# Kernel tuning notes

Hardware: AMD Instinct MI355X
Metric: run time of the kernel (lower is better)

The kernel has to match this reference:

```python
import jax, jax.numpy as jnp
import numpy as np

LORA_RANK = 16
LORA_ALPHA = 32
CHUNK_SIZE = 256
TTT_LR = 0.01
CLIP_THRESHOLD = 1.0
SCALING = LORA_ALPHA / LORA_RANK
LN_EPS = 1e-5


def setup_inputs() -> dict:
    key = jax.random.key(0)
    ks = jax.random.split(key, 5)
    B, S, K, H = 2, 8192, 1024, 1024
    x = jax.random.normal(ks[0], (B, S, K), dtype=jnp.float32)
    Wb = jax.random.normal(ks[1], (H, K), dtype=jnp.float32) / np.sqrt(K)
    init_A = jax.random.normal(ks[2], (H, LORA_RANK), dtype=jnp.float32) * 0.01
    init_B = jax.random.normal(ks[3], (LORA_RANK, K), dtype=jnp.float32) * 0.01
    ln_gamma = jnp.ones((K,), dtype=jnp.float32)
    ln_beta = jnp.zeros((K,), dtype=jnp.float32)
    Wp = jax.random.normal(ks[4], (H, K), dtype=jnp.float32) / np.sqrt(K)
    return {"x": x, "Wb": Wb, "init_A": init_A, "init_B": init_B,
            "ln_gamma": ln_gamma, "ln_beta": ln_beta, "Wp": Wp}


def _forward(x, Wb, init_A, init_B, ln_gamma, ln_beta, Wp):
    B_sz, Seq, k_dim = x.shape
    h_dim = Wb.shape[0]
    r = init_A.shape[1]
    nc = Seq // CHUNK_SIZE  # Seq chosen divisible; pad_len == 0

    base_out = x @ Wb.T  # [B, S, H]

    # --- target construction under no_grad: LayerNorm + left-shift ---
    xd = jax.lax.stop_gradient(x)
    mu = jnp.mean(xd, axis=-1, keepdims=True)
    var = jnp.mean((xd - mu) ** 2, axis=-1, keepdims=True)
    xn = (xd - mu) * jax.lax.rsqrt(var + LN_EPS) * ln_gamma + ln_beta
    shifted = jnp.pad(xn[:, 1:, :], ((0, 0), (0, 1), (0, 0)))
    shifted = jax.lax.stop_gradient(shifted)

    V = shifted @ Wp.T  # [B, S, H]

    Z = x.reshape(B_sz * nc, CHUNK_SIZE, k_dim)
    Vc = V.reshape(B_sz * nc, CHUNK_SIZE, h_dim)

    # per-chunk fast-weight deltas
    proj_in = Z @ init_B.T                                # [BC, C, r]
    dA = jnp.einsum('bch,bcr->bhr', Vc, proj_in)          # [BC, H, r]
    proj_err = Vc @ init_A                                # [BC, C, r]
    dB = jnp.einsum('bcr,bck->brk', proj_err, Z)          # [BC, r, K]

    dA = dA.reshape(B_sz, nc, h_dim, r)
    dB = dB.reshape(B_sz, nc, r, k_dim)

    # exclusive cross-chunk cumsum
    accA = jnp.cumsum(dA, axis=1)
    accB = jnp.cumsum(dB, axis=1)
    accA = jnp.concatenate([jnp.zeros_like(accA[:, :1]), accA[:, :-1]], axis=1)
    accB = jnp.concatenate([jnp.zeros_like(accB[:, :1]), accB[:, :-1]], axis=1)

    lr = TTT_LR * SCALING
    rawA = (lr * accA).reshape(-1, h_dim, r)
    rawB = (lr * accB).reshape(-1, r, k_dim)

    # joint norm clip (norm_type=2)
    norm_sq = (jnp.sum(rawA.astype(jnp.float32) ** 2, axis=(-2, -1), keepdims=True)
               + jnp.sum(rawB.astype(jnp.float32) ** 2, axis=(-2, -1), keepdims=True))
    total_norm = jnp.sqrt(norm_sq)
    coef = jnp.minimum(CLIP_THRESHOLD / (total_norm + 1e-6), 1.0).astype(rawA.dtype)

    A_eff = init_A[None] - rawA * coef  # [BC, H, r]
    B_eff = init_B[None] - rawB * coef  # [BC, r, K]

    mid = jnp.einsum('bck,brk->bcr', Z, B_eff)          # [BC, C, r]
    lora = jnp.einsum('bcr,bhr->bch', mid, A_eff)       # [BC, C, H]
    lora = lora.reshape(B_sz, Seq, h_dim)

    return base_out + lora * SCALING


def reference(x, Wb, init_A, init_B, ln_gamma, ln_beta, Wp):
    return _forward(x, Wb, init_A, init_B, ln_gamma, ln_beta, Wp)
```

## Files before the change

### kernel.cpp

```cpp
#include <hip/hip_runtime.h>

typedef __attribute__((ext_vector_type(8))) short s16x8;
typedef __attribute__((ext_vector_type(4))) float f32x4;
typedef __attribute__((ext_vector_type(2))) float f32x2;
typedef unsigned short u16;

#define B_SZ 2
#define SEQ 8192
#define KD 1024
#define HD 1024
#define RK 16
#define CH 256
#define NCH 64
static constexpr float LR_SC = 0.02f;
static constexpr float SCALE_OUT = 2.0f;

__device__ __forceinline__ u16 f2b(float f) {
  union { float f; unsigned int u; } c; c.f = f;
  unsigned int u = c.u;
  unsigned int r = (u + 0x7fffu + ((u >> 16) & 1u)) >> 16;
  return (u16)r;
}
__device__ __forceinline__ float b2f(u16 v) {
  union { unsigned int u; float f; } c; c.u = ((unsigned int)v) << 16; return c.f;
}
__device__ __forceinline__ void async16(const u16* g, u16* l) {
  __builtin_amdgcn_global_load_lds((const __attribute__((address_space(1))) void*)g,
                                   (__attribute__((address_space(3))) void*)l, 16, 0, 0);
}

__global__ __launch_bounds__(256) void cvt_all(const float* __restrict__ Wb,
                                               const float* __restrict__ Wp,
                                               const float* __restrict__ initB,
                                               u16* __restrict__ Wbb,
                                               u16* __restrict__ Wpb,
                                               u16* __restrict__ iBb) {
  int bid = blockIdx.x;
  const float* src; u16* dst; int base;
  if (bid < 1024)      { src = Wb;    dst = Wbb; base = bid; }
  else if (bid < 2048) { src = Wp;    dst = Wpb; base = bid - 1024; }
  else                 { src = initB; dst = iBb; base = bid - 2048; }
  int i = (base * 256 + threadIdx.x) * 4;
  float4 v = *(const float4*)(src + i);
  ushort4 o; o.x = f2b(v.x); o.y = f2b(v.y); o.z = f2b(v.z); o.w = f2b(v.w);
  *(ushort4*)(dst + i) = o;
}

__global__ __launch_bounds__(256) void wpat_part(const float* __restrict__ initA,
                                                 const float* __restrict__ Wp,
                                                 float* __restrict__ part) {
  int t = threadIdx.x;
  int k = blockIdx.x * 256 + t;
  int hseg = blockIdx.y;
  __shared__ float Asm[64 * 16];
  *(float4*)&Asm[t * 4] = *(const float4*)&initA[(size_t)hseg * 1024 + t * 4];
  __syncthreads();
  float acc[16];
  #pragma unroll
  for (int j = 0; j < 16; j++) acc[j] = 0.f;
  const float* wp = Wp + (size_t)hseg * 64 * KD + k;
  #pragma unroll 8
  for (int hh = 0; hh < 64; hh++) {
    float w = wp[(size_t)hh * KD];
    const float4* ar = (const float4*)&Asm[hh * 16];
    #pragma unroll
    for (int qq = 0; qq < 4; qq++) {
      float4 a = ar[qq];
      acc[qq*4+0] += w * a.x; acc[qq*4+1] += w * a.y;
      acc[qq*4+2] += w * a.z; acc[qq*4+3] += w * a.w;
    }
  }
  float* o = part + ((size_t)hseg * 1024 + k) * 16;
  #pragma unroll
  for (int qq = 0; qq < 4; qq++) {
    float4 r; r.x = acc[qq*4]; r.y = acc[qq*4+1]; r.z = acc[qq*4+2]; r.w = acc[qq*4+3];
    *(float4*)&o[qq * 4] = r;
  }
}

__global__ __launch_bounds__(256) void wpat_reduce(const float* __restrict__ part,
                                                   u16* __restrict__ WpAT) {
  int idx = blockIdx.x * 256 + threadIdx.x;
  int k = idx & 1023, r = idx >> 10;
  float s = 0.f;
  #pragma unroll
  for (int seg = 0; seg < 16; seg++)
    s += part[((size_t)seg * 1024 + k) * 16 + r];
  WpAT[(size_t)r * KD + k] = f2b(s);
}

__global__ __launch_bounds__(256) void ln_shift(const float* __restrict__ x,
                                                const float* __restrict__ gamma,
                                                const float* __restrict__ beta,
                                                u16* __restrict__ xb,
                                                u16* __restrict__ shb) {
  int row = blockIdx.x;
  int t = threadIdx.x;
  int s = row & (SEQ - 1);
  const float* xr = x + (size_t)row * KD;
  float4 v = *(const float4*)(xr + t * 4);
  ushort4 o; o.x = f2b(v.x); o.y = f2b(v.y); o.z = f2b(v.z); o.w = f2b(v.w);
  *(ushort4*)(xb + (size_t)row * KD + t * 4) = o;

  if (s == 0) {
    ushort4 z; z.x = 0; z.y = 0; z.z = 0; z.w = 0;
    *(ushort4*)(shb + ((size_t)row + SEQ - 1) * KD + t * 4) = z;
    return;
  }
  float s1 = v.x + v.y + v.z + v.w;
  float s2 = v.x * v.x + v.y * v.y + v.z * v.z + v.w * v.w;
  #pragma unroll
  for (int off = 32; off > 0; off >>= 1) {
    s1 += __shfl_down(s1, off);
    s2 += __shfl_down(s2, off);
  }
  __shared__ float red[8];
  int wave = t >> 6, lane = t & 63;
  if (lane == 0) { red[wave * 2] = s1; red[wave * 2 + 1] = s2; }
  __syncthreads();
  float sum = red[0] + red[2] + red[4] + red[6];
  float ssq = red[1] + red[3] + red[5] + red[7];
  float mu = sum * (1.0f / KD);
  float var = ssq * (1.0f / KD) - mu * mu;
  float rstd = rsqrtf(var + 1e-5f);
  float4 g = *(const float4*)(gamma + t * 4);
  float4 bb = *(const float4*)(beta + t * 4);
  ushort4 so;
  so.x = f2b((v.x - mu) * rstd * g.x + bb.x);
  so.y = f2b((v.y - mu) * rstd * g.y + bb.y);
  so.z = f2b((v.z - mu) * rstd * g.z + bb.z);
  so.w = f2b((v.w - mu) * rstd * g.w + bb.w);
  *(ushort4*)(shb + (size_t)(row - 1) * KD + t * 4) = so;
}

__global__ __launch_bounds__(256, 2) void gemm_fused(const u16* __restrict__ A,
                                                     const u16* __restrict__ Bm,
                                                     const u16* __restrict__ mid2,
                                                     const u16* __restrict__ Aef,
                                                     float* __restrict__ C) {
  constexpr int BM = 128, BN = 128, BK = 64, N = HD, Kd = KD;
  __shared__ __align__(16) char SMEMRAW[64 * 132 * 4];
  u16* As = (u16*)SMEMRAW;
  u16* Bs = (u16*)(SMEMRAW + BM * BK * 2);
  float* SM = (float*)SMEMRAW;
  int tid = threadIdx.x;
  int lane = tid & 63, wave = tid >> 6;
  int lb = blockIdx.x + 8 * blockIdx.y;
  int q = lb & 7, t = lb >> 3;
  int mb = q * 16 + (t >> 3);
  int nb = t & 7;
  int m0 = mb * 128, n0 = nb * 128;
  int wm = (wave >> 1) * 64, wn = (wave & 1) * 64;
  int lr = lane & 15;
  int qd = lane >> 4;
  int sw = lr & 7;
  int slot0 = ((qd ^ sw) * 8);
  int slot1 = (((4 + qd) ^ sw) * 8);
  f32x4 acc[4][4] = {};

  const u16* gbase; u16* lbase;
  if (wave < 2) { gbase = A + (size_t)(m0 + wave * 64) * Kd; lbase = As + wave * 64 * BK; }
  else          { gbase = Bm + (size_t)(n0 + (wave - 2) * 64) * Kd; lbase = Bs + (wave - 2) * 64 * BK; }
  int srow = lane >> 3;
  int scol = ((lane & 7) ^ srow) * 8;
  const u16* gsrc = gbase + (size_t)srow * Kd + scol;

  for (int k0 = 0; k0 < Kd; k0 += BK) {
    #pragma unroll
    for (int i = 0; i < 8; i++)
      async16(gsrc + (size_t)i * 8 * Kd, lbase + i * 512);
    gsrc += BK;
    __syncthreads();
    s16x8 af[4], bfr[4];
    #pragma unroll
    for (int i = 0; i < 4; i++) af[i] = *(const s16x8*)(As + (wm + i * 16 + lr) * BK + slot0);
    #pragma unroll
    for (int j = 0; j < 4; j++) bfr[j] = *(const s16x8*)(Bs + (wn + j * 16 + lr) * BK + slot0);
    #pragma unroll
    for (int i = 0; i < 4; i++)
      #pragma unroll
      for (int j = 0; j < 4; j++)
        acc[i][j] = __builtin_amdgcn_mfma_f32_16x16x32_bf16(af[i], bfr[j], acc[i][j], 0, 0, 0);
    #pragma unroll
    for (int i = 0; i < 4; i++) af[i] = *(const s16x8*)(As + (wm + i * 16 + lr) * BK + slot1);
    #pragma unroll
    for (int j = 0; j < 4; j++) bfr[j] = *(const s16x8*)(Bs + (wn + j * 16 + lr) * BK + slot1);
    #pragma unroll
    for (int i = 0; i < 4; i++)
      #pragma unroll
      for (int j = 0; j < 4; j++)
        acc[i][j] = __builtin_amdgcn_mfma_f32_16x16x32_bf16(af[i], bfr[j], acc[i][j], 0, 0, 0);
    __syncthreads();
  }

  {
    int chunk = m0 >> 8;
    const u16* abase = Aef + (size_t)chunk * (HD * RK);
    int klane = lane >> 4;
    s16x8 am2[4], bn2[4];
    #pragma unroll
    for (int i = 0; i < 4; i++) {
      if (klane < 2)
        am2[i] = *(const s16x8*)(mid2 + (size_t)(m0 + wm + i * 16 + lr) * RK + klane * 8);
      else { s16x8 z = {}; am2[i] = z; }
    }
    #pragma unroll
    for (int j = 0; j < 4; j++) {
      if (klane < 2)
        bn2[j] = *(const s16x8*)(abase + (size_t)(n0 + wn + j * 16 + lr) * RK + klane * 8);
      else { s16x8 z = {}; bn2[j] = z; }
    }
    #pragma unroll
    for (int i = 0; i < 4; i++)
      #pragma unroll
      for (int j = 0; j < 4; j++)
        acc[i][j] = __builtin_amdgcn_mfma_f32_16x16x32_bf16(am2[i], bn2[j], acc[i][j], 0, 0, 0);
  }

  int rb = qd * 4, cc = lr;
  int row8 = tid >> 3;
  int fidx = tid & 7;
  #pragma unroll
  for (int h = 0; h < 2; h++) {
    __syncthreads();
    if ((wave >> 1) == h) {
      #pragma unroll
      for (int i = 0; i < 4; i++)
        #pragma unroll
        for (int j = 0; j < 4; j++)
          #pragma unroll
          for (int p = 0; p < 4; p++)
            SM[(i * 16 + rb + p) * 132 + wn + j * 16 + cc] = acc[i][j][p];
    }
    __syncthreads();
    #pragma unroll
    for (int s = 0; s < 2; s++) {
      int rl = s * 32 + row8;
      const float* src = SM + rl * 132 + fidx * 4;
      float* dst = C + (size_t)(m0 + h * 64 + rl) * N + n0 + fidx * 4;
      #pragma unroll
      for (int qq = 0; qq < 4; qq++)
        *(float4*)(dst + qq * 32) = *(const float4*)(src + qq * 32);
    }
  }
}

__global__ __launch_bounds__(256) void rank16_proj(const u16* __restrict__ xb,
                                                   const u16* __restrict__ shb,
                                                   const u16* __restrict__ iBb,
                                                   const u16* __restrict__ WpAT,
                                                   float* __restrict__ pin,
                                                   float* __restrict__ per) {
  const u16* X; const u16* W; float* O;
  if (blockIdx.z == 0) { X = xb; W = iBb; O = pin; }
  else                 { X = shb; W = WpAT; O = per; }
  int wave = threadIdx.x >> 6, lane = threadIdx.x & 63;
  int m0 = (blockIdx.x * 4 + wave) * 16;
  int lr = lane & 15, lk = (lane >> 4) * 8;
  const u16* xp = X + (size_t)(m0 + lr) * KD + lk;
  const u16* wp = W + (size_t)lr * KD + lk;
  f32x4 acc = {};
  #pragma unroll 8
  for (int k0 = 0; k0 < KD; k0 += 32) {
    s16x8 a = *(const s16x8*)xp;
    s16x8 b = *(const s16x8*)wp;
    acc = __builtin_amdgcn_mfma_f32_16x16x32_bf16(a, b, acc, 0, 0, 0);
    xp += 32; wp += 32;
  }
  int rb = (lane >> 4) * 4, cc = lane & 15;
  #pragma unroll
  for (int p = 0; p < 4; p++)
    O[(size_t)(m0 + rb + p) * RK + cc] = acc[p];
}

__global__ __launch_bounds__(256) void rank16_mid(const u16* __restrict__ xb,
                                                  const u16* __restrict__ Bef,
                                                  u16* __restrict__ mid2) {
  int wave = threadIdx.x >> 6, lane = threadIdx.x & 63;
  int m0 = (blockIdx.x * 4 + wave) * 16;
  int chunk = m0 >> 8;
  int lr = lane & 15, lk = (lane >> 4) * 8;
  const u16* xp = xb + (size_t)(m0 + lr) * KD + lk;
  const u16* wp = Bef + (size_t)chunk * (RK * KD) + (size_t)lr * KD + lk;
  f32x4 acc = {};
  #pragma unroll 8
  for (int k0 = 0; k0 < KD; k0 += 32) {
    s16x8 a = *(const s16x8*)xp;
    s16x8 b = *(const s16x8*)wp;
    acc = __builtin_amdgcn_mfma_f32_16x16x32_bf16(a, b, acc, 0, 0, 0);
    xp += 32; wp += 32;
  }
  int rb = (lane >> 4) * 4, cc = lane & 15;
  #pragma unroll
  for (int p = 0; p < 4; p++)
    mid2[(size_t)(m0 + rb + p) * RK + cc] = f2b(SCALE_OUT * acc[p]);
}

__global__ __launch_bounds__(256) void gk_kernel(const u16* __restrict__ xb,
                                                 const u16* __restrict__ shb,
                                                 const float* __restrict__ pin,
                                                 const float* __restrict__ per,
                                                 float* __restrict__ G,
                                                 float* __restrict__ dB) {
  int tile = blockIdx.x;
  int chunk = blockIdx.y;
  int which = blockIdx.z;
  int t = threadIdx.x;
  __shared__ float P[CH * RK];
  const float* psrc = which ? per : pin;
  for (int i = t; i < 1024; i += 256)
    *(float4*)&P[i * 4] = *(const float4*)&psrc[(size_t)chunk * 4096 + i * 4];
  __syncthreads();
  f32x2 acc[8];
  #pragma unroll
  for (int j = 0; j < 8; j++) acc[j] = (f32x2){0.f, 0.f};
  int col = tile * 256 + t;
  const u16* src = (which ? xb : shb) + (size_t)chunk * CH * KD + col;
  #pragma unroll 4
  for (int c = 0; c < 256; c++) {
    float v = b2f(src[(size_t)c * 1024]);
    f32x2 vv = {v, v};
    const f32x2* pr = (const f32x2*)&P[c * 16];
    #pragma unroll
    for (int qq = 0; qq < 8; qq++)
      acc[qq] += vv * pr[qq];
  }
  float* o = (which ? dB : G) + (size_t)chunk * 16384 + col;
  #pragma unroll
  for (int j = 0; j < 8; j++) {
    o[(size_t)(2 * j) * 1024] = acc[j][0];
    o[(size_t)(2 * j + 1) * 1024] = acc[j][1];
  }
}

__global__ __launch_bounds__(256) void cumsum_kernel(const float* __restrict__ G,
                                                     const float* __restrict__ dB,
                                                     u16* __restrict__ rawG,
                                                     float* __restrict__ rawB) {
  int idx = blockIdx.x * 256 + threadIdx.x;
  int which = idx >> 15;
  int rem = idx & 32767;
  int b = rem >> 14;
  int e = rem & 16383;
  size_t base = (size_t)b * 32 * 16384 + e;
  if (which == 0) {
    float run = 0.f;
    #pragma unroll 8
    for (int i = 0; i < 32; i++) {
      size_t off = base + (size_t)i * 16384;
      float nv = G[off];
      rawG[off] = f2b(LR_SC * run);
      run += nv;
    }
  } else {
    float run = 0.f;
    #pragma unroll 8
    for (int i = 0; i < 32; i++) {
      size_t off = base + (size_t)i * 16384;
      float nv = dB[off];
      rawB[off] = LR_SC * run;
      run += nv;
    }
  }
}

__global__ __launch_bounds__(256) void dagemm(const u16* __restrict__ Wpb,
                                              const u16* __restrict__ rawG,
                                              float* __restrict__ rawA) {
  int wave = threadIdx.x >> 6, lane = threadIdx.x & 63;
  int m0 = (blockIdx.x * 4 + wave) * 16;
  int chunk = blockIdx.y;
  int lr = lane & 15, lk = (lane >> 4) * 8;
  const u16* ap = Wpb + (size_t)(m0 + lr) * KD + lk;
  const u16* bp = rawG + (size_t)chunk * 16384 + (size_t)lr * KD + lk;
  f32x4 acc = {};
  #pragma unroll 8
  for (int k0 = 0; k0 < KD; k0 += 32) {
    s16x8 a = *(const s16x8*)ap;
    s16x8 b = *(const s16x8*)bp;
    acc = __builtin_amdgcn_mfma_f32_16x16x32_bf16(a, b, acc, 0, 0, 0);
    ap += 32; bp += 32;
  }
  int rb = (lane >> 4) * 4, cc = lane & 15;
  #pragma unroll
  for (int p = 0; p < 4; p++)
    rawA[(size_t)chunk * 16384 + (size_t)(m0 + rb + p) * RK + cc] = acc[p];
}

__global__ __launch_bounds__(256) void coef_norm(const float* __restrict__ rawA,
                                                 const float* __restrict__ rawB,
                                                 float* __restrict__ part) {
  int b = blockIdx.x;
  int chunk = b >> 2, quarter = b & 3;
  size_t base = (size_t)chunk * 16384 + quarter * 4096;
  const float* a = rawA + base;
  const float* bb = rawB + base;
  int t = threadIdx.x;
  float s = 0.f;
  #pragma unroll
  for (int i = 0; i < 4; i++) {
    float4 v = *(const float4*)(a + (i * 256 + t) * 4);
    s += v.x*v.x + v.y*v.y + v.z*v.z + v.w*v.w;
    float4 w = *(const float4*)(bb + (i * 256 + t) * 4);
    s += w.x*w.x + w.y*w.y + w.z*w.z + w.w*w.w;
  }
  #pragma unroll
  for (int off = 32; off > 0; off >>= 1) s += __shfl_down(s, off);
  __shared__ float red[4];
  int wave = t >> 6, lane = t & 63;
  if (lane == 0) red[wave] = s;
  __syncthreads();
  if (t == 0) part[b] = red[0] + red[1] + red[2] + red[3];
}

__global__ __launch_bounds__(256) void coef_emit(const float* __restrict__ initA,
                                                 const float* __restrict__ initB,
                                                 const float* __restrict__ rawA,
                                                 const float* __restrict__ rawB,
                                                 const float* __restrict__ part,
                                                 u16* __restrict__ Aef,
                                                 u16* __restrict__ Bef) {
  int b = blockIdx.x;
  int chunk = b >> 3, eighth = b & 7;
  float tot = part[chunk * 4] + part[chunk * 4 + 1] + part[chunk * 4 + 2] + part[chunk * 4 + 3];
  float cf = fminf(1.0f / (sqrtf(tot) + 1e-6f), 1.0f);
  size_t cbase = (size_t)chunk * 16384;
  int t = threadIdx.x;
  #pragma unroll
  for (int i = 0; i < 2; i++) {
    int idx = eighth * 2048 + (i * 256 + t) * 4;
    float4 iv = *(const float4*)(initA + idx);
    float4 rv = *(const float4*)(rawA + cbase + idx);
    ushort4 r;
    r.x = f2b(iv.x - rv.x * cf); r.y = f2b(iv.y - rv.y * cf);
    r.z = f2b(iv.z - rv.z * cf); r.w = f2b(iv.w - rv.w * cf);
    *(ushort4*)(Aef + cbase + idx) = r;
    float4 iw = *(const float4*)(initB + idx);
    float4 rw = *(const float4*)(rawB + cbase + idx);
    ushort4 rr;
    rr.x = f2b(iw.x - rw.x * cf); rr.y = f2b(iw.y - rw.y * cf);
    rr.z = f2b(iw.z - rw.z * cf); rr.w = f2b(iw.w - rw.w * cf);
    *(ushort4*)(Bef + cbase + idx) = rr;
  }
}

extern "C" void kernel_launch(void* const* d_in, const int* in_sizes, int n_in,
                              void* d_out, int out_size, void* d_ws, size_t ws_size,
                              hipStream_t stream) {
  (void)in_sizes; (void)n_in; (void)out_size; (void)ws_size;
  const float* x     = (const float*)d_in[0];
  const float* Wb    = (const float*)d_in[1];
  const float* initA = (const float*)d_in[2];
  const float* initB = (const float*)d_in[3];
  const float* gamma = (const float*)d_in[4];
  const float* beta  = (const float*)d_in[5];
  const float* Wp    = (const float*)d_in[6];
  float* out = (float*)d_out;

  char* ws = (char*)d_ws;
  size_t off = 0;
  auto alloc = [&](size_t bytes) -> void* {
    void* p = ws + off;
    off = (off + bytes + 255) & ~(size_t)255;
    return p;
  };
  const size_t ROWS = (size_t)B_SZ * SEQ;
  u16* xb    = (u16*)alloc(ROWS * KD * 2);
  u16* shb   = (u16*)alloc(ROWS * KD * 2);
  u16* Wbb   = (u16*)alloc((size_t)HD * KD * 2);
  u16* Wpb   = (u16*)alloc((size_t)HD * KD * 2);
  u16* iBb   = (u16*)alloc((size_t)RK * KD * 2);
  u16* WpAT  = (u16*)alloc((size_t)RK * KD * 2);
  float* wpart = (float*)alloc((size_t)16 * KD * RK * 4);
  float* pin = (float*)alloc((size_t)NCH * CH * RK * 4);
  float* per = (float*)alloc((size_t)NCH * CH * RK * 4);
  float* G   = (float*)alloc((size_t)NCH * 16384 * 4);
  float* dB  = (float*)alloc((size_t)NCH * 16384 * 4);
  u16* rawG  = (u16*)alloc((size_t)NCH * 16384 * 2);
  float* rawB= (float*)alloc((size_t)NCH * 16384 * 4);
  float* rawA= (float*)alloc((size_t)NCH * 16384 * 4);
  u16* Aef   = (u16*)alloc((size_t)NCH * 16384 * 2);
  u16* Bef   = (u16*)alloc((size_t)NCH * 16384 * 2);
  u16* mid2  = (u16*)alloc(ROWS * RK * 2);
  float* npart = (float*)alloc((size_t)256 * 4);

  cvt_all<<<2064, 256, 0, stream>>>(Wb, Wp, initB, Wbb, Wpb, iBb);
  wpat_part<<<dim3(4, 16), 256, 0, stream>>>(initA, Wp, wpart);
  wpat_reduce<<<64, 256, 0, stream>>>(wpart, WpAT);
  ln_shift<<<ROWS, 256, 0, stream>>>(x, gamma, beta, xb, shb);
  rank16_proj<<<dim3(256, 1, 2), 256, 0, stream>>>(xb, shb, iBb, WpAT, pin, per);
  gk_kernel<<<dim3(4, NCH, 2), 256, 0, stream>>>(xb, shb, pin, per, G, dB);
  cumsum_kernel<<<256, 256, 0, stream>>>(G, dB, rawG, rawB);
  dagemm<<<dim3(16, NCH), 256, 0, stream>>>(Wpb, rawG, rawA);
  coef_norm<<<256, 256, 0, stream>>>(rawA, rawB, npart);
  coef_emit<<<512, 256, 0, stream>>>(initA, initB, rawA, rawB, npart, Aef, Bef);
  rank16_mid<<<256, 256, 0, stream>>>(xb, Bef, mid2);
  gemm_fused<<<dim3(8, 128), 256, 0, stream>>>(xb, Wbb, mid2, Aef, out);
}
```

Before: 285.4 us.

## Use one wave per row in LayerNorm, dual MFMA accumulators, batched cumsum loads

LayerNorm/shift now processes one row per wavefront with 16 floats per lane and a pure shuffle reduction, removing the shared-memory reduction and block barrier and quartering the block count. The rank-16 MFMA loops split into two independent accumulators to break the dependency chain. The cumsum kernel preloads all 32 values before the scan to expose memory-level parallelism, and gk_kernel's unroll goes from 4 to 8. Register pressure rises in several kernels.

```diff
diff --git a/kernel.cpp b/kernel.cpp
--- a/kernel.cpp
+++ b/kernel.cpp
@@ -27,6 +27,10 @@
 __device__ __forceinline__ void async16(const u16* g, u16* l) {
   __builtin_amdgcn_global_load_lds((const __attribute__((address_space(1))) void*)g,
                                    (__attribute__((address_space(3))) void*)l, 16, 0, 0);
+}
+__device__ __forceinline__ ushort4 cvt4(float4 v) {
+  ushort4 o; o.x = f2b(v.x); o.y = f2b(v.y); o.z = f2b(v.z); o.w = f2b(v.w);
+  return o;
 }
 
 __global__ __launch_bounds__(256) void cvt_all(const float* __restrict__ Wb,
@@ -42,8 +46,7 @@
   else                 { src = initB; dst = iBb; base = bid - 2048; }
   int i = (base * 256 + threadIdx.x) * 4;
   float4 v = *(const float4*)(src + i);
-  ushort4 o; o.x = f2b(v.x); o.y = f2b(v.y); o.z = f2b(v.z); o.w = f2b(v.w);
-  *(ushort4*)(dst + i) = o;
+  *(ushort4*)(dst + i) = cvt4(v);
 }
 
 __global__ __launch_bounds__(256) void wpat_part(const float* __restrict__ initA,
@@ -94,43 +97,64 @@
                                                 const float* __restrict__ beta,
                                                 u16* __restrict__ xb,
                                                 u16* __restrict__ shb) {
-  int row = blockIdx.x;
-  int t = threadIdx.x;
+  int wave = threadIdx.x >> 6, lane = threadIdx.x & 63;
+  int row = blockIdx.x * 4 + wave;
   int s = row & (SEQ - 1);
-  const float* xr = x + (size_t)row * KD;
-  float4 v = *(const float4*)(xr + t * 4);
-  ushort4 o; o.x = f2b(v.x); o.y = f2b(v.y); o.z = f2b(v.z); o.w = f2b(v.w);
-  *(ushort4*)(xb + (size_t)row * KD + t * 4) = o;
+  int col = lane * 16;
+  const float* xr = x + (size_t)row * KD + col;
+  float4 v0 = *(const float4*)(xr + 0);
+  float4 v1 = *(const float4*)(xr + 4);
+  float4 v2 = *(const float4*)(xr + 8);
+  float4 v3 = *(const float4*)(xr + 12);
+  u16* xo = xb + (size_t)row * KD + col;
+  *(ushort4*)(xo + 0)  = cvt4(v0);
+  *(ushort4*)(xo + 4)  = cvt4(v1);
+  *(ushort4*)(xo + 8)  = cvt4(v2);
+  *(ushort4*)(xo + 12) = cvt4(v3);
 
   if (s == 0) {
     ushort4 z; z.x = 0; z.y = 0; z.z = 0; z.w = 0;
-    *(ushort4*)(shb + ((size_t)row + SEQ - 1) * KD + t * 4) = z;
+    u16* zo = shb + ((size_t)row + SEQ - 1) * KD + col;
+    *(ushort4*)(zo + 0) = z; *(ushort4*)(zo + 4) = z;
+    *(ushort4*)(zo + 8) = z; *(ushort4*)(zo + 12) = z;
     return;
   }
-  float s1 = v.x + v.y + v.z + v.w;
-  float s2 = v.x * v.x + v.y * v.y + v.z * v.z + v.w * v.w;
+  float s1 = v0.x+v0.y+v0.z+v0.w + v1.x+v1.y+v1.z+v1.w
+           + v2.x+v2.y+v2.z+v2.w + v3.x+v3.y+v3.z+v3.w;
+  float s2 = v0.x*v0.x+v0.y*v0.y+v0.z*v0.z+v0.w*v0.w
+           + v1.x*v1.x+v1.y*v1.y+v1.z*v1.z+v1.w*v1.w
+           + v2.x*v2.x+v2.y*v2.y+v2.z*v2.z+v2.w*v2.w
+           + v3.x*v3.x+v3.y*v3.y+v3.z*v3.z+v3.w*v3.w;
   #pragma unroll
   for (int off = 32; off > 0; off >>= 1) {
-    s1 += __shfl_down(s1, off);
-    s2 += __shfl_down(s2, off);
-  }
-  __shared__ float red[8];
-  int wave = t >> 6, lane = t & 63;
-  if (lane == 0) { red[wave * 2] = s1; red[wave * 2 + 1] = s2; }
-  __syncthreads();
-  float sum = red[0] + red[2] + red[4] + red[6];
-  float ssq = red[1] + red[3] + red[5] + red[7];
-  float mu = sum * (1.0f / KD);
-  float var = ssq * (1.0f / KD) - mu * mu;
+    s1 += __shfl_xor(s1, off);
+    s2 += __shfl_xor(s2, off);
+  }
+  float mu = s1 * (1.0f / KD);
+  float var = s2 * (1.0f / KD) - mu * mu;
   float rstd = rsqrtf(var + 1e-5f);
-  float4 g = *(const float4*)(gamma + t * 4);
-  float4 bb = *(const float4*)(beta + t * 4);
-  ushort4 so;
-  so.x = f2b((v.x - mu) * rstd * g.x + bb.x);
-  so.y = f2b((v.y - mu) * rstd * g.y + bb.y);
-  so.z = f2b((v.z - mu) * rstd * g.z + bb.z);
-  so.w = f2b((v.w - mu) * rstd * g.w + bb.w);
-  *(ushort4*)(shb + (size_t)(row - 1) * KD + t * 4) = so;
+  float4 g0 = *(const float4*)(gamma + col + 0);
+  float4 g1 = *(const float4*)(gamma + col + 4);
+  float4 g2 = *(const float4*)(gamma + col + 8);
+  float4 g3 = *(const float4*)(gamma + col + 12);
+  float4 b0 = *(const float4*)(beta + col + 0);
+  float4 b1 = *(const float4*)(beta + col + 4);
+  float4 b2 = *(const float4*)(beta + col + 8);
+  float4 b3 = *(const float4*)(beta + col + 12);
+  u16* so = shb + (size_t)(row - 1) * KD + col;
+  float4 r;
+  r.x=(v0.x-mu)*rstd*g0.x+b0.x; r.y=(v0.y-mu)*rstd*g0.y+b0.y;
+  r.z=(v0.z-mu)*rstd*g0.z+b0.z; r.w=(v0.w-mu)*rstd*g0.w+b0.w;
+  *(ushort4*)(so + 0) = cvt4(r);
+  r.x=(v1.x-mu)*rstd*g1.x+b1.x; r.y=(v1.y-mu)*rstd*g1.y+b1.y;
+  r.z=(v1.z-mu)*rstd*g1.z+b1.z; r.w=(v1.w-mu)*rstd*g1.w+b1.w;
+  *(ushort4*)(so + 4) = cvt4(r);
+  r.x=(v2.x-mu)*rstd*g2.x+b2.x; r.y=(v2.y-mu)*rstd*g2.y+b2.y;
+  r.z=(v2.z-mu)*rstd*g2.z+b2.z; r.w=(v2.w-mu)*rstd*g2.w+b2.w;
+  *(ushort4*)(so + 8) = cvt4(r);
+  r.x=(v3.x-mu)*rstd*g3.x+b3.x; r.y=(v3.y-mu)*rstd*g3.y+b3.y;
+  r.z=(v3.z-mu)*rstd*g3.z+b3.z; r.w=(v3.w-mu)*rstd*g3.w+b3.w;
+  *(ushort4*)(so + 12) = cvt4(r);
 }
 
 __global__ __launch_bounds__(256, 2) void gemm_fused(const u16* __restrict__ A,
@@ -259,14 +283,16 @@
   int lr = lane & 15, lk = (lane >> 4) * 8;
   const u16* xp = X + (size_t)(m0 + lr) * KD + lk;
   const u16* wp = W + (size_t)lr * KD + lk;
-  f32x4 acc = {};
+  f32x4 acc0 = {}, acc1 = {};
   #pragma unroll 8
-  for (int k0 = 0; k0 < KD; k0 += 32) {
-    s16x8 a = *(const s16x8*)xp;
-    s16x8 b = *(const s16x8*)wp;
-    acc = __builtin_amdgcn_mfma_f32_16x16x32_bf16(a, b, acc, 0, 0, 0);
-    xp += 32; wp += 32;
-  }
+  for (int k0 = 0; k0 < KD; k0 += 64) {
+    acc0 = __builtin_amdgcn_mfma_f32_16x16x32_bf16(*(const s16x8*)xp,
+                                                   *(const s16x8*)wp, acc0, 0, 0, 0);
+    acc1 = __builtin_amdgcn_mfma_f32_16x16x32_bf16(*(const s16x8*)(xp + 32),
+                                                   *(const s16x8*)(wp + 32), acc1, 0, 0, 0);
+    xp += 64; wp += 64;
+  }
+  f32x4 acc = acc0 + acc1;
   int rb = (lane >> 4) * 4, cc = lane & 15;
   #pragma unroll
   for (int p = 0; p < 4; p++)
@@ -282,14 +308,16 @@
   int lr = lane & 15, lk = (lane >> 4) * 8;
   const u16* xp = xb + (size_t)(m0 + lr) * KD + lk;
   const u16* wp = Bef + (size_t)chunk * (RK * KD) + (size_t)lr * KD + lk;
-  f32x4 acc = {};
+  f32x4 acc0 = {}, acc1 = {};
   #pragma unroll 8
-  for (int k0 = 0; k0 < KD; k0 += 32) {
-    s16x8 a = *(const s16x8*)xp;
-    s16x8 b = *(const s16x8*)wp;
-    acc = __builtin_amdgcn_mfma_f32_16x16x32_bf16(a, b, acc, 0, 0, 0);
-    xp += 32; wp += 32;
-  }
+  for (int k0 = 0; k0 < KD; k0 += 64) {
+    acc0 = __builtin_amdgcn_mfma_f32_16x16x32_bf16(*(const s16x8*)xp,
+                                                   *(const s16x8*)wp, acc0, 0, 0, 0);
+    acc1 = __builtin_amdgcn_mfma_f32_16x16x32_bf16(*(const s16x8*)(xp + 32),
+                                                   *(const s16x8*)(wp + 32), acc1, 0, 0, 0);
+    xp += 64; wp += 64;
+  }
+  f32x4 acc = acc0 + acc1;
   int rb = (lane >> 4) * 4, cc = lane & 15;
   #pragma unroll
   for (int p = 0; p < 4; p++)
@@ -316,7 +344,7 @@
   for (int j = 0; j < 8; j++) acc[j] = (f32x2){0.f, 0.f};
   int col = tile * 256 + t;
   const u16* src = (which ? xb : shb) + (size_t)chunk * CH * KD + col;
-  #pragma unroll 4
+  #pragma unroll 8
   for (int c = 0; c < 256; c++) {
     float v = b2f(src[(size_t)c * 1024]);
     f32x2 vv = {v, v};
@@ -344,22 +372,24 @@
   int e = rem & 16383;
   size_t base = (size_t)b * 32 * 16384 + e;
   if (which == 0) {
+    float v[32];
+    #pragma unroll
+    for (int i = 0; i < 32; i++) v[i] = G[base + (size_t)i * 16384];
     float run = 0.f;
-    #pragma unroll 8
+    #pragma unroll
     for (int i = 0; i < 32; i++) {
-      size_t off = base + (size_t)i * 16384;
-      float nv = G[off];
-      rawG[off] = f2b(LR_SC * run);
-      run += nv;
+      rawG[base + (size_t)i * 16384] = f2b(LR_SC * run);
+      run += v[i];
     }
   } else {
+    float v[32];
+    #pragma unroll
+    for (int i = 0; i < 32; i++) v[i] = dB[base + (size_t)i * 16384];
     float run = 0.f;
-    #pragma unroll 8
+    #pragma unroll
     for (int i = 0; i < 32; i++) {
-      size_t off = base + (size_t)i * 16384;
-      float nv = dB[off];
-      rawB[off] = LR_SC * run;
-      run += nv;
+      rawB[base + (size_t)i * 16384] = LR_SC * run;
+      run += v[i];
     }
   }
 }
@@ -373,14 +403,16 @@
   int lr = lane & 15, lk = (lane >> 4) * 8;
   const u16* ap = Wpb + (size_t)(m0 + lr) * KD + lk;
   const u16* bp = rawG + (size_t)chunk * 16384 + (size_t)lr * KD + lk;
-  f32x4 acc = {};
+  f32x4 acc0 = {}, acc1 = {};
   #pragma unroll 8
-  for (int k0 = 0; k0 < KD; k0 += 32) {
-    s16x8 a = *(const s16x8*)ap;
-    s16x8 b = *(const s16x8*)bp;
-    acc = __builtin_amdgcn_mfma_f32_16x16x32_bf16(a, b, acc, 0, 0, 0);
-    ap += 32; bp += 32;
-  }
+  for (int k0 = 0; k0 < KD; k0 += 64) {
+    acc0 = __builtin_amdgcn_mfma_f32_16x16x32_bf16(*(const s16x8*)ap,
+                                                   *(const s16x8*)bp, acc0, 0, 0, 0);
+    acc1 = __builtin_amdgcn_mfma_f32_16x16x32_bf16(*(const s16x8*)(ap + 32),
+                                                   *(const s16x8*)(bp + 32), acc1, 0, 0, 0);
+    ap += 64; bp += 64;
+  }
+  f32x4 acc = acc0 + acc1;
   int rb = (lane >> 4) * 4, cc = lane & 15;
   #pragma unroll
   for (int p = 0; p < 4; p++)
@@ -431,16 +463,16 @@
     int idx = eighth * 2048 + (i * 256 + t) * 4;
     float4 iv = *(const float4*)(initA + idx);
     float4 rv = *(const float4*)(rawA + cbase + idx);
-    ushort4 r;
-    r.x = f2b(iv.x - rv.x * cf); r.y = f2b(iv.y - rv.y * cf);
-    r.z = f2b(iv.z - rv.z * cf); r.w = f2b(iv.w - rv.w * cf);
-    *(ushort4*)(Aef + cbase + idx) = r;
+    float4 r;
+    r.x = iv.x - rv.x * cf; r.y = iv.y - rv.y * cf;
+    r.z = iv.z - rv.z * cf; r.w = iv.w - rv.w * cf;
+    *(ushort4*)(Aef + cbase + idx) = cvt4(r);
     float4 iw = *(const float4*)(initB + idx);
     float4 rw = *(const float4*)(rawB + cbase + idx);
-    ushort4 rr;
-    rr.x = f2b(iw.x - rw.x * cf); rr.y = f2b(iw.y - rw.y * cf);
-    rr.z = f2b(iw.z - rw.z * cf); rr.w = f2b(iw.w - rw.w * cf);
-    *(ushort4*)(Bef + cbase + idx) = rr;
+    float4 rr;
+    rr.x = iw.x - rw.x * cf; rr.y = iw.y - rw.y * cf;
+    rr.z = iw.z - rw.z * cf; rr.w = iw.w - rw.w * cf;
+    *(ushort4*)(Bef + cbase + idx) = cvt4(rr);
   }
 }
 
@@ -487,7 +519,7 @@
   cvt_all<<<2064, 256, 0, stream>>>(Wb, Wp, initB, Wbb, Wpb, iBb);
   wpat_part<<<dim3(4, 16), 256, 0, stream>>>(initA, Wp, wpart);
   wpat_reduce<<<64, 256, 0, stream>>>(wpart, WpAT);
-  ln_shift<<<ROWS, 256, 0, stream>>>(x, gamma, beta, xb, shb);
+  ln_shift<<<4096, 256, 0, stream>>>(x, gamma, beta, xb, shb);
   rank16_proj<<<dim3(256, 1, 2), 256, 0, stream>>>(xb, shb, iBb, WpAT, pin, per);
   gk_kernel<<<dim3(4, NCH, 2), 256, 0, stream>>>(xb, shb, pin, per, G, dB);
   cumsum_kernel<<<256, 256, 0, stream>>>(G, dB, rawG, rawB);
```

New measurement: 290.8 us. Within noise of the previous version (+1.9%).
